# Performance work log

Measured on AMD Instinct MI355X. Metric: run time of the kernel, lower is better.

## Reference

```python
import jax, jax.numpy as jnp
import numpy as np

DEPTH = 64
N_HEAD = 8
FF = 128
EPS = 1e-5


def layer_norm(x, g, b):
    mu = jnp.mean(x, axis=-1, keepdims=True)
    var = jnp.mean((x - mu) ** 2, axis=-1, keepdims=True)
    return (x - mu) * jax.lax.rsqrt(var + EPS) * g + b


def setup_inputs() -> dict:
    key = jax.random.key(0)
    ks = jax.random.split(key, 16)
    B, S, d, h = 4, 512, DEPTH, N_HEAD
    s = 1.0 / np.sqrt(d)
    return {
        "seq": jax.random.normal(ks[0], (B, S, d), jnp.float32),
        "pos_enc": jax.random.normal(ks[1], (B, S, S, d), jnp.float32),
        "Wq": jax.random.normal(ks[2], (d, d * h), jnp.float32) * s,
        "Wk": jax.random.normal(ks[3], (d, d * h), jnp.float32) * s,
        "Wv": jax.random.normal(ks[4], (d, d * h), jnp.float32) * s,
        "Wo": jax.random.normal(ks[5], (d * h, d), jnp.float32) / np.sqrt(d * h),
        "Wp": jax.random.normal(ks[6], (d, h), jnp.float32) * s,
        "bp": jnp.zeros((h,), jnp.float32),
        "W1": jax.random.normal(ks[7], (d, FF), jnp.float32) * s,
        "b1": jnp.zeros((FF,), jnp.float32),
        "W2": jax.random.normal(ks[8], (FF, d), jnp.float32) / np.sqrt(FF),
        "b2": jnp.zeros((d,), jnp.float32),
        "g_att": jnp.ones((d,), jnp.float32),
        "b_att": jnp.zeros((d,), jnp.float32),
        "g_ff": jnp.ones((d,), jnp.float32),
        "b_ff": jnp.zeros((d,), jnp.float32),
    }


def reference(seq, pos_enc, Wq, Wk, Wv, Wo, Wp, bp, W1, b1, W2, b2, g_att, b_att, g_ff, b_ff):
    B, S, d = seq.shape
    h = N_HEAD
    # QKV: [B,S,h,d] -> [B,h,S,d]; head_dim == depth in this module
    q = (seq @ Wq).reshape(B, S, h, d).transpose(0, 2, 1, 3)
    k = (seq @ Wk).reshape(B, S, h, d).transpose(0, 2, 1, 3)
    v = (seq @ Wv).reshape(B, S, h, d).transpose(0, 2, 1, 3)
    a = jnp.einsum('bhid,bhjd->bhij', q, k) / jnp.sqrt(jnp.asarray(d, seq.dtype))
    # additive learned positional bias: [B,S,S,d] @ [d,h] -> [B,S,S,h] -> [B,h,S,S]
    p = jnp.einsum('bijd,dh->bhij', pos_enc, Wp) + bp[None, :, None, None]
    a = jax.nn.softmax(a + p, axis=-1)
    heads = jnp.einsum('bhij,bhjd->bhid', a, v)  # [B,h,S,d]
    o = heads.transpose(0, 2, 1, 3).reshape(B, S, h * d) @ Wo
    x = layer_norm(seq + o, g_att, b_att)
    y = jax.nn.relu(x @ W1 + b1) @ W2 + b2
    return layer_norm(x + y, g_ff, b_ff)
```

## Files before the change

kernel.cpp:

```cpp
#include <hip/hip_runtime.h>
#include <hip/hip_bf16.h>

#define DEPTH 64
#define NH 8
#define SEQL 512
#define BATCH 4
#define FFDIM 128
#define PROJ (DEPTH*NH)
#define LOG2E 1.44269504088896340736f

typedef __hip_bfloat16 bf16;
typedef __attribute__((ext_vector_type(8))) short short8;
typedef __attribute__((ext_vector_type(4))) float floatx4;

__device__ __forceinline__ short f2bs(float f) {
    __hip_bfloat16 h = __float2bfloat16(f);
    return *reinterpret_cast<short*>(&h);
}
__device__ __forceinline__ float bs2f(short s) {
    __hip_bfloat16 h = *reinterpret_cast<__hip_bfloat16*>(&s);
    return __bfloat162float(h);
}

__global__ __launch_bounds__(256) void front_kernel(
    const float* __restrict__ seq, const float* __restrict__ Wq,
    const float* __restrict__ Wk, const float* __restrict__ Wv,
    const float* __restrict__ pos, const float* __restrict__ Wp,
    const float* __restrict__ bp,
    bf16* __restrict__ q, bf16* __restrict__ k, bf16* __restrict__ vT,
    bf16* __restrict__ p)
{
    __shared__ __align__(16) union {
        struct { short sS[64][72]; short sW[128][72]; } g;
        struct { float sW2[4][132]; float sb[8]; } pb;
    } U;
    int t = threadIdx.x;
    int bid = blockIdx.x;

    if (bid < 384) {
        int lane = t & 63, w = t >> 6;
        int z = bid >> 7, rem = bid & 127;
        int mi = rem & 31, ni = rem >> 5;
        const float* W; int vflag = 0; bf16* out;
        if (z == 0)      { W = Wq; out = q; }
        else if (z == 1) { W = Wk; out = k; }
        else             { W = Wv; out = vT; vflag = 1; }
        int m0 = mi * 64;
        int n0 = ni * 128;

        for (int idx = t; idx < 4096; idx += 256) {
            int r = idx >> 6, kk = idx & 63;
            U.g.sS[r][kk] = f2bs(seq[(long)(m0 + r)*64 + kk]);
        }
        for (int idx = t; idx < 8192; idx += 256) {
            int kk = idx >> 7, n = idx & 127;
            U.g.sW[n][kk] = f2bs(W[kk*512 + n0 + n]);
        }
        __syncthreads();

        int ln = lane & 15, g4 = lane >> 4;
        int mt = w;
        floatx4 acc[2][4];
        #pragma unroll
        for (int nh = 0; nh < 2; nh++)
            #pragma unroll
            for (int nt = 0; nt < 4; nt++) acc[nh][nt] = (floatx4){0.f,0.f,0.f,0.f};
        #pragma unroll
        for (int ks = 0; ks < 2; ks++) {
            short8 af = *(const short8*)&U.g.sS[mt*16 + ln][ks*32 + g4*8];
            #pragma unroll
            for (int nh = 0; nh < 2; nh++)
                #pragma unroll
                for (int nt = 0; nt < 4; nt++) {
                    short8 bfv = *(const short8*)&U.g.sW[nh*64 + nt*16 + ln][ks*32 + g4*8];
                    acc[nh][nt] = __builtin_amdgcn_mfma_f32_16x16x32_bf16(af, bfv, acc[nh][nt], 0, 0, 0);
                }
        }

        if (!vflag) {
            #pragma unroll
            for (int nh = 0; nh < 2; nh++)
                #pragma unroll
                for (int nt = 0; nt < 4; nt++)
                    #pragma unroll
                    for (int r = 0; r < 4; r++) {
                        int grow = m0 + mt*16 + g4*4 + r;
                        int col  = n0 + nh*64 + nt*16 + ln;
                        int b = grow >> 9, s = grow & 511;
                        int h = col >> 6, d = col & 63;
                        out[(((long)(b*8 + h)*512) + s)*64 + d] = __float2bfloat16(acc[nh][nt][r]);
                    }
        } else {
            __syncthreads();
            short (*sT)[72] = U.g.sW;
            #pragma unroll
            for (int nh = 0; nh < 2; nh++)
                #pragma unroll
                for (int nt = 0; nt < 4; nt++)
                    #pragma unroll
                    for (int r = 0; r < 4; r++)
                        sT[nh*64 + nt*16 + ln][mt*16 + g4*4 + r] = f2bs(acc[nh][nt][r]);
            __syncthreads();
            int b = m0 >> 9, s0 = m0 & 511;
            for (int idx = t; idx < 1024; idx += 256) {
                int lc = idx >> 3, c8 = idx & 7;
                *(uint4*)(out + ((long)(b*512 + n0 + lc))*512 + s0 + c8*8) =
                    *(const uint4*)&sT[lc][c8*8];
            }
        }
    } else {
        int pid = bid - 384;
        for (int i = t; i < 512; i += 256) {
            int sub = i >> 7, rest = i & 127;
            int lk = rest >> 3, h = rest & 7;
            int kk = ((lk >> 2) << 4) + sub*4 + (lk & 3);
            U.pb.sW2[sub][lk*8 + h] = Wp[kk*8 + h];
        }
        if (t < 8) U.pb.sb[t] = bp[t];
        __syncthreads();

        int sub = t & 3;
        int lrow = t >> 2;
        long row = (long)pid*64 + lrow;

        const float4* src = (const float4*)(pos + row*64);
        float4 ch[4];
        #pragma unroll
        for (int i = 0; i < 4; i++) ch[i] = src[i*4 + sub];

        float acc[8];
        #pragma unroll
        for (int h = 0; h < 8; h++) acc[h] = 0.f;
        #pragma unroll
        for (int i = 0; i < 4; i++) {
            #pragma unroll
            for (int e = 0; e < 4; e++) {
                float x = ((const float*)&ch[i])[e];
                int lk = i*4 + e;
                const float4* wr = (const float4*)&U.pb.sW2[sub][lk*8];
                float4 wa = wr[0], wb = wr[1];
                acc[0] += x*wa.x; acc[1] += x*wa.y; acc[2] += x*wa.z; acc[3] += x*wa.w;
                acc[4] += x*wb.x; acc[5] += x*wb.y; acc[6] += x*wb.z; acc[7] += x*wb.w;
            }
        }
        #pragma unroll
        for (int h = 0; h < 8; h++) {
            acc[h] += __shfl_xor(acc[h], 1, 64);
            acc[h] += __shfl_xor(acc[h], 2, 64);
        }
        int b = (int)(row >> 18);
        int rem = (int)(row & 262143);
        int i = rem >> 9, j = rem & 511;
        int h1 = sub, h2 = sub + 4;
        p[(((long)(b*8 + h1)*512 + i) << 9) + j] = __float2bfloat16(acc[h1] + U.pb.sb[h1]);
        p[(((long)(b*8 + h2)*512 + i) << 9) + j] = __float2bfloat16(acc[h2] + U.pb.sb[h2]);
    }
}

__global__ __launch_bounds__(128) void attn_kernel(
    const bf16* __restrict__ q, const bf16* __restrict__ k,
    const bf16* __restrict__ vT, const bf16* __restrict__ p,
    bf16* __restrict__ heads)
{
    __shared__ __align__(16) short sQ[32*72];
    __shared__ __align__(16) short sK[64*72];
    __shared__ __align__(16) short sV[64*72];
    __shared__ __align__(16) short sP[2][16*72];

    int t = threadIdx.x;
    int lane = t & 63, w = t >> 6;
    int bid = blockIdx.x;
    int it = bid & 15;
    int bh = bid >> 4;
    int i0 = it*32;

    const bf16* qb = q + ((long)bh*SEQL + i0)*DEPTH;
    const bf16* kb = k + (long)bh*SEQL*DEPTH;
    const bf16* vb = vT + (long)bh*DEPTH*SEQL;
    const bf16* pb = p + ((long)bh*SEQL + i0)*SEQL;

    for (int c = t; c < 256; c += 128) {
        int r = c >> 3, c8 = c & 7;
        *(uint4*)((char*)sQ + r*144 + c8*16) = *(const uint4*)(qb + r*64 + c8*8);
    }

    int ln = lane & 15, g4 = lane >> 4;
    float lsum[4];
    floatx4 oacc[4];
    #pragma unroll
    for (int r = 0; r < 4; r++) lsum[r] = 0.f;
    #pragma unroll
    for (int ds = 0; ds < 4; ds++) oacc[ds] = (floatx4){0.f,0.f,0.f,0.f};

    unsigned short pf[16];
    #pragma unroll
    for (int js = 0; js < 4; js++)
        #pragma unroll
        for (int r = 0; r < 4; r++)
            pf[js*4 + r] = *(const unsigned short*)&pb[(long)(w*16 + g4*4 + r)*SEQL + js*16 + ln];

    #pragma unroll
    for (int jt = 0; jt < 8; jt++) {
        __syncthreads();
        int j0 = jt*64;
        for (int c = t; c < 512; c += 128) {
            int r = c >> 3, c8 = c & 7;
            *(uint4*)((char*)sK + r*144 + c8*16) = *(const uint4*)(kb + (long)(j0 + r)*64 + c8*8);
        }
        for (int c = t; c < 512; c += 128) {
            int r = c >> 3, c8 = c & 7;
            *(uint4*)((char*)sV + r*144 + c8*16) = *(const uint4*)(vb + (long)r*512 + j0 + c8*8);
        }
        __syncthreads();

        unsigned short cur[16];
        #pragma unroll
        for (int e = 0; e < 16; e++) cur[e] = pf[e];
        if (jt < 7) {
            int jn = (jt + 1)*64;
            #pragma unroll
            for (int js = 0; js < 4; js++)
                #pragma unroll
                for (int r = 0; r < 4; r++)
                    pf[js*4 + r] = *(const unsigned short*)&pb[(long)(w*16 + g4*4 + r)*SEQL + jn + js*16 + ln];
        }

        floatx4 sacc[4];
        #pragma unroll
        for (int js = 0; js < 4; js++) sacc[js] = (floatx4){0.f,0.f,0.f,0.f};
        #pragma unroll
        for (int kk = 0; kk < 2; kk++) {
            short8 aq = *(const short8*)((const char*)sQ + (w*16 + ln)*144 + kk*64 + g4*16);
            #pragma unroll
            for (int js = 0; js < 4; js++) {
                short8 bk = *(const short8*)((const char*)sK + (js*16 + ln)*144 + kk*64 + g4*16);
                sacc[js] = __builtin_amdgcn_mfma_f32_16x16x32_bf16(aq, bk, sacc[js], 0, 0, 0);
            }
        }
        #pragma unroll
        for (int js = 0; js < 4; js++)
            #pragma unroll
            for (int r = 0; r < 4; r++) {
                float pv = bs2f((short)cur[js*4 + r]);
                float e = exp2f((sacc[js][r]*0.125f + pv)*LOG2E);
                lsum[r] += e;
                sP[w][(g4*4 + r)*72 + js*16 + ln] = f2bs(e);
            }
        #pragma unroll
        for (int kk = 0; kk < 2; kk++) {
            short8 ap = *(const short8*)((const char*)sP[w] + ln*144 + kk*64 + g4*16);
            #pragma unroll
            for (int ds = 0; ds < 4; ds++) {
                short8 bv = *(const short8*)((const char*)sV + (ds*16 + ln)*144 + kk*64 + g4*16);
                oacc[ds] = __builtin_amdgcn_mfma_f32_16x16x32_bf16(ap, bv, oacc[ds], 0, 0, 0);
            }
        }
    }

    #pragma unroll
    for (int r = 0; r < 4; r++)
        #pragma unroll
        for (int m = 1; m < 16; m <<= 1) lsum[r] += __shfl_xor(lsum[r], m, 64);

    int b = bh >> 3, h = bh & 7;
    #pragma unroll
    for (int ds = 0; ds < 4; ds++)
        #pragma unroll
        for (int r = 0; r < 4; r++) {
            float val = oacc[ds][r] / lsum[r];
            int gi = i0 + w*16 + g4*4 + r;
            int col = h*64 + ds*16 + ln;
            heads[((long)b*SEQL + gi)*PROJ + col] = __float2bfloat16(val);
        }
}

__global__ __launch_bounds__(256) void tail_kernel(
    const bf16* __restrict__ heads, const float* __restrict__ Wo,
    const float* __restrict__ seq, const float* __restrict__ g_att,
    const float* __restrict__ b_att, const float* __restrict__ W1,
    const float* __restrict__ b1, const float* __restrict__ W2,
    const float* __restrict__ b2, const float* __restrict__ g_ff,
    const float* __restrict__ b_ff, float* __restrict__ out)
{
    __shared__ __align__(16) short sH[8][520];
    __shared__ float sX[8][68];
    __shared__ float sHid[8][132];
    int t = threadIdx.x;
    int w = t >> 6, lane = t & 63;
    long g0 = (long)blockIdx.x*8;

    for (int idx = t; idx < 512; idx += 256) {
        int r = idx >> 6, c8 = idx & 63;
        *(uint4*)((char*)&sH[r][0] + c8*16) = *(const uint4*)(heads + (g0 + r)*PROJ + c8*8);
    }
    __syncthreads();

    int r0 = w*2, r1 = w*2 + 1;
    float acc0 = 0.f, acc1 = 0.f;
    #pragma unroll 4
    for (int kk8 = 0; kk8 < 64; kk8++) {
        short8 a0 = *(const short8*)&sH[r0][kk8*8];
        short8 a1 = *(const short8*)&sH[r1][kk8*8];
        #pragma unroll
        for (int e = 0; e < 8; e++) {
            float wv = Wo[(kk8*8 + e)*DEPTH + lane];
            acc0 += bs2f(a0[e])*wv;
            acc1 += bs2f(a1[e])*wv;
        }
    }
    float ga = g_att[lane], ba = b_att[lane];
    float xn[2];
    #pragma unroll
    for (int rr = 0; rr < 2; rr++) {
        long row = g0 + w*2 + rr;
        float x0 = (rr ? acc1 : acc0) + seq[row*DEPTH + lane];
        float s1 = x0, s2 = x0*x0;
        #pragma unroll
        for (int m = 1; m < 64; m <<= 1) { s1 += __shfl_xor(s1, m, 64); s2 += __shfl_xor(s2, m, 64); }
        float mu = s1*(1.f/64.f);
        float var = s2*(1.f/64.f) - mu*mu;
        float rstd = rsqrtf(var + 1e-5f);
        xn[rr] = (x0 - mu)*rstd*ga + ba;
        sX[w*2 + rr][lane] = xn[rr];
    }

    float b1a = b1[lane], b1b = b1[lane + 64];
    float h00 = b1a, h01 = b1b, h10 = b1a, h11 = b1b;
    #pragma unroll 4
    for (int kk = 0; kk < DEPTH; kk++) {
        float w0 = W1[kk*FFDIM + lane];
        float w1 = W1[kk*FFDIM + 64 + lane];
        float x0v = sX[r0][kk], x1v = sX[r1][kk];
        h00 += x0v*w0; h01 += x0v*w1;
        h10 += x1v*w0; h11 += x1v*w1;
    }
    sHid[r0][lane] = fmaxf(h00, 0.f); sHid[r0][lane + 64] = fmaxf(h01, 0.f);
    sHid[r1][lane] = fmaxf(h10, 0.f); sHid[r1][lane + 64] = fmaxf(h11, 0.f);

    float bb = b2[lane];
    float acc20 = bb, acc21 = bb;
    #pragma unroll 4
    for (int kk = 0; kk < FFDIM; kk++) {
        float wv = W2[kk*DEPTH + lane];
        acc20 += sHid[r0][kk]*wv;
        acc21 += sHid[r1][kk]*wv;
    }
    float gf = g_ff[lane], bf = b_ff[lane];
    #pragma unroll
    for (int rr = 0; rr < 2; rr++) {
        long row = g0 + w*2 + rr;
        float z = xn[rr] + (rr ? acc21 : acc20);
        float t1 = z, t2 = z*z;
        #pragma unroll
        for (int m = 1; m < 64; m <<= 1) { t1 += __shfl_xor(t1, m, 64); t2 += __shfl_xor(t2, m, 64); }
        float mu2 = t1*(1.f/64.f);
        float var2 = t2*(1.f/64.f) - mu2*mu2;
        float rstd2 = rsqrtf(var2 + 1e-5f);
        out[row*DEPTH + lane] = (z - mu2)*rstd2*gf + bf;
    }
}

extern "C" void kernel_launch(void* const* d_in, const int* in_sizes, int n_in,
                              void* d_out, int out_size, void* d_ws, size_t ws_size,
                              hipStream_t stream) {
    const float* seq   = (const float*)d_in[0];
    const float* pos   = (const float*)d_in[1];
    const float* Wq    = (const float*)d_in[2];
    const float* Wk    = (const float*)d_in[3];
    const float* Wv    = (const float*)d_in[4];
    const float* Wo    = (const float*)d_in[5];
    const float* Wp    = (const float*)d_in[6];
    const float* bp    = (const float*)d_in[7];
    const float* W1    = (const float*)d_in[8];
    const float* b1    = (const float*)d_in[9];
    const float* W2    = (const float*)d_in[10];
    const float* b2    = (const float*)d_in[11];
    const float* g_att = (const float*)d_in[12];
    const float* b_att = (const float*)d_in[13];
    const float* g_ff  = (const float*)d_in[14];
    const float* b_ff  = (const float*)d_in[15];
    float* outp = (float*)d_out;

    bf16* qb  = (bf16*)d_ws;
    bf16* kb  = qb + 1048576;
    bf16* vTb = kb + 1048576;
    bf16* pb  = vTb + 1048576;
    bf16* hb  = pb + 8388608;

    front_kernel<<<16768, 256, 0, stream>>>(seq, Wq, Wk, Wv, pos, Wp, bp,
                                            qb, kb, vTb, pb);
    attn_kernel <<<512,   128, 0, stream>>>(qb, kb, vTb, pb, hb);
    tail_kernel <<<256,   256, 0, stream>>>(hb, Wo, seq, g_att, b_att,
                                            W1, b1, W2, b2, g_ff, b_ff, outp);
}
```

Measured before the change: 121.3 us.

## Split front kernel, store positional bias head-interleaved, widen attention tiles

Splits the fused front kernel into separate QKV and positional-bias kernels. The bias kernel now handles two rows per thread and writes all 8 heads as one 16-byte vector in a [B,S,S,h] layout, replacing scattered 2-byte stores. The attention kernel reads that interleaved layout with a stride of 8 and now uses 64-row query tiles with 4 waves. The aim is to cut the store cost of writing the large bias tensor. The trade-off is that attention gathers the bias with strided 2-byte loads, and there is one extra kernel launch.

```diff
diff --git a/kernel.cpp b/kernel.cpp
--- a/kernel.cpp
+++ b/kernel.cpp
@@ -22,164 +22,174 @@
     return __bfloat162float(h);
 }
 
-__global__ __launch_bounds__(256) void front_kernel(
+__global__ __launch_bounds__(256) void qkv_kernel(
     const float* __restrict__ seq, const float* __restrict__ Wq,
     const float* __restrict__ Wk, const float* __restrict__ Wv,
+    bf16* __restrict__ q, bf16* __restrict__ k, bf16* __restrict__ vT)
+{
+    __shared__ __align__(16) short sS[64][72];
+    __shared__ __align__(16) short sW[128][72];
+    __shared__ __align__(16) short sT[128][72];
+    int t = threadIdx.x;
+    int lane = t & 63, w = t >> 6;
+    const float* W; int vflag = 0;
+    bf16* out;
+    if (blockIdx.z == 0)      { W = Wq; out = q; }
+    else if (blockIdx.z == 1) { W = Wk; out = k; }
+    else                      { W = Wv; out = vT; vflag = 1; }
+    int m0 = blockIdx.x * 64;
+    int n0 = blockIdx.y * 128;
+
+    for (int idx = t; idx < 4096; idx += 256) {
+        int r = idx >> 6, kk = idx & 63;
+        sS[r][kk] = f2bs(seq[(long)(m0 + r)*64 + kk]);
+    }
+    for (int idx = t; idx < 8192; idx += 256) {
+        int kk = idx >> 7, n = idx & 127;
+        sW[n][kk] = f2bs(W[kk*512 + n0 + n]);
+    }
+    __syncthreads();
+
+    int ln = lane & 15, g4 = lane >> 4;
+    int mt = w;
+    floatx4 acc[2][4];
+    #pragma unroll
+    for (int nh = 0; nh < 2; nh++)
+        #pragma unroll
+        for (int nt = 0; nt < 4; nt++) acc[nh][nt] = (floatx4){0.f,0.f,0.f,0.f};
+    #pragma unroll
+    for (int ks = 0; ks < 2; ks++) {
+        short8 af = *(const short8*)&sS[mt*16 + ln][ks*32 + g4*8];
+        #pragma unroll
+        for (int nh = 0; nh < 2; nh++)
+            #pragma unroll
+            for (int nt = 0; nt < 4; nt++) {
+                short8 bfv = *(const short8*)&sW[nh*64 + nt*16 + ln][ks*32 + g4*8];
+                acc[nh][nt] = __builtin_amdgcn_mfma_f32_16x16x32_bf16(af, bfv, acc[nh][nt], 0, 0, 0);
+            }
+    }
+
+    if (!vflag) {
+        #pragma unroll
+        for (int nh = 0; nh < 2; nh++)
+            #pragma unroll
+            for (int nt = 0; nt < 4; nt++)
+                #pragma unroll
+                for (int r = 0; r < 4; r++) {
+                    int grow = m0 + mt*16 + g4*4 + r;
+                    int col  = n0 + nh*64 + nt*16 + ln;
+                    int b = grow >> 9, s = grow & 511;
+                    int h = col >> 6, d = col & 63;
+                    out[(((long)(b*8 + h)*512) + s)*64 + d] = __float2bfloat16(acc[nh][nt][r]);
+                }
+    } else {
+        #pragma unroll
+        for (int nh = 0; nh < 2; nh++)
+            #pragma unroll
+            for (int nt = 0; nt < 4; nt++)
+                #pragma unroll
+                for (int r = 0; r < 4; r++)
+                    sT[nh*64 + nt*16 + ln][mt*16 + g4*4 + r] = f2bs(acc[nh][nt][r]);
+        __syncthreads();
+        int b = m0 >> 9, s0 = m0 & 511;
+        for (int idx = t; idx < 1024; idx += 256) {
+            int lc = idx >> 3, c8 = idx & 7;
+            *(uint4*)(out + ((long)(b*512 + n0 + lc))*512 + s0 + c8*8) =
+                *(const uint4*)&sT[lc][c8*8];
+        }
+    }
+}
+
+__global__ __launch_bounds__(256, 8) void pbias_kernel(
     const float* __restrict__ pos, const float* __restrict__ Wp,
-    const float* __restrict__ bp,
-    bf16* __restrict__ q, bf16* __restrict__ k, bf16* __restrict__ vT,
-    bf16* __restrict__ p)
+    const float* __restrict__ bp, bf16* __restrict__ p)
 {
-    __shared__ __align__(16) union {
-        struct { short sS[64][72]; short sW[128][72]; } g;
-        struct { float sW2[4][132]; float sb[8]; } pb;
-    } U;
+    __shared__ __align__(16) float sW2[4][132];
+    __shared__ float sb[8];
     int t = threadIdx.x;
-    int bid = blockIdx.x;
-
-    if (bid < 384) {
-        int lane = t & 63, w = t >> 6;
-        int z = bid >> 7, rem = bid & 127;
-        int mi = rem & 31, ni = rem >> 5;
-        const float* W; int vflag = 0; bf16* out;
-        if (z == 0)      { W = Wq; out = q; }
-        else if (z == 1) { W = Wk; out = k; }
-        else             { W = Wv; out = vT; vflag = 1; }
-        int m0 = mi * 64;
-        int n0 = ni * 128;
-
-        for (int idx = t; idx < 4096; idx += 256) {
-            int r = idx >> 6, kk = idx & 63;
-            U.g.sS[r][kk] = f2bs(seq[(long)(m0 + r)*64 + kk]);
-        }
-        for (int idx = t; idx < 8192; idx += 256) {
-            int kk = idx >> 7, n = idx & 127;
-            U.g.sW[n][kk] = f2bs(W[kk*512 + n0 + n]);
-        }
-        __syncthreads();
-
-        int ln = lane & 15, g4 = lane >> 4;
-        int mt = w;
-        floatx4 acc[2][4];
-        #pragma unroll
-        for (int nh = 0; nh < 2; nh++)
-            #pragma unroll
-            for (int nt = 0; nt < 4; nt++) acc[nh][nt] = (floatx4){0.f,0.f,0.f,0.f};
-        #pragma unroll
-        for (int ks = 0; ks < 2; ks++) {
-            short8 af = *(const short8*)&U.g.sS[mt*16 + ln][ks*32 + g4*8];
-            #pragma unroll
-            for (int nh = 0; nh < 2; nh++)
-                #pragma unroll
-                for (int nt = 0; nt < 4; nt++) {
-                    short8 bfv = *(const short8*)&U.g.sW[nh*64 + nt*16 + ln][ks*32 + g4*8];
-                    acc[nh][nt] = __builtin_amdgcn_mfma_f32_16x16x32_bf16(af, bfv, acc[nh][nt], 0, 0, 0);
-                }
-        }
-
-        if (!vflag) {
-            #pragma unroll
-            for (int nh = 0; nh < 2; nh++)
-                #pragma unroll
-                for (int nt = 0; nt < 4; nt++)
-                    #pragma unroll
-                    for (int r = 0; r < 4; r++) {
-                        int grow = m0 + mt*16 + g4*4 + r;
-                        int col  = n0 + nh*64 + nt*16 + ln;
-                        int b = grow >> 9, s = grow & 511;
-                        int h = col >> 6, d = col & 63;
-                        out[(((long)(b*8 + h)*512) + s)*64 + d] = __float2bfloat16(acc[nh][nt][r]);
-                    }
-        } else {
-            __syncthreads();
-            short (*sT)[72] = U.g.sW;
-            #pragma unroll
-            for (int nh = 0; nh < 2; nh++)
-                #pragma unroll
-                for (int nt = 0; nt < 4; nt++)
-                    #pragma unroll
-                    for (int r = 0; r < 4; r++)
-                        sT[nh*64 + nt*16 + ln][mt*16 + g4*4 + r] = f2bs(acc[nh][nt][r]);
-            __syncthreads();
-            int b = m0 >> 9, s0 = m0 & 511;
-            for (int idx = t; idx < 1024; idx += 256) {
-                int lc = idx >> 3, c8 = idx & 7;
-                *(uint4*)(out + ((long)(b*512 + n0 + lc))*512 + s0 + c8*8) =
-                    *(const uint4*)&sT[lc][c8*8];
-            }
-        }
-    } else {
-        int pid = bid - 384;
-        for (int i = t; i < 512; i += 256) {
-            int sub = i >> 7, rest = i & 127;
-            int lk = rest >> 3, h = rest & 7;
-            int kk = ((lk >> 2) << 4) + sub*4 + (lk & 3);
-            U.pb.sW2[sub][lk*8 + h] = Wp[kk*8 + h];
-        }
-        if (t < 8) U.pb.sb[t] = bp[t];
-        __syncthreads();
-
-        int sub = t & 3;
-        int lrow = t >> 2;
-        long row = (long)pid*64 + lrow;
-
-        const float4* src = (const float4*)(pos + row*64);
-        float4 ch[4];
-        #pragma unroll
-        for (int i = 0; i < 4; i++) ch[i] = src[i*4 + sub];
-
-        float acc[8];
-        #pragma unroll
-        for (int h = 0; h < 8; h++) acc[h] = 0.f;
-        #pragma unroll
-        for (int i = 0; i < 4; i++) {
-            #pragma unroll
-            for (int e = 0; e < 4; e++) {
-                float x = ((const float*)&ch[i])[e];
-                int lk = i*4 + e;
-                const float4* wr = (const float4*)&U.pb.sW2[sub][lk*8];
-                float4 wa = wr[0], wb = wr[1];
-                acc[0] += x*wa.x; acc[1] += x*wa.y; acc[2] += x*wa.z; acc[3] += x*wa.w;
-                acc[4] += x*wb.x; acc[5] += x*wb.y; acc[6] += x*wb.z; acc[7] += x*wb.w;
-            }
-        }
+    for (int i = t; i < 512; i += 256) {
+        int sub = i >> 7, rest = i & 127;
+        int lk = rest >> 3, h = rest & 7;
+        int kk = ((lk >> 2) << 4) + sub*4 + (lk & 3);
+        sW2[sub][lk*8 + h] = Wp[kk*8 + h];
+    }
+    if (t < 8) sb[t] = bp[t];
+    __syncthreads();
+
+    int sub = t & 3;
+    int lr = t >> 2;
+    long rowA = (long)blockIdx.x*128 + lr;
+    long rowB = rowA + 64;
+
+    const float4* srcA = (const float4*)(pos + rowA*64);
+    const float4* srcB = (const float4*)(pos + rowB*64);
+    float4 chA[4], chB[4];
+    #pragma unroll
+    for (int i = 0; i < 4; i++) chA[i] = srcA[i*4 + sub];
+    #pragma unroll
+    for (int i = 0; i < 4; i++) chB[i] = srcB[i*4 + sub];
+
+    float accA[8], accB[8];
+    #pragma unroll
+    for (int h = 0; h < 8; h++) { accA[h] = 0.f; accB[h] = 0.f; }
+    #pragma unroll
+    for (int i = 0; i < 4; i++) {
+        #pragma unroll
+        for (int e = 0; e < 4; e++) {
+            int lk = i*4 + e;
+            const float4* wr = (const float4*)&sW2[sub][lk*8];
+            float4 wa = wr[0], wb = wr[1];
+            float xA = ((const float*)&chA[i])[e];
+            float xB = ((const float*)&chB[i])[e];
+            accA[0] += xA*wa.x; accA[1] += xA*wa.y; accA[2] += xA*wa.z; accA[3] += xA*wa.w;
+            accA[4] += xA*wb.x; accA[5] += xA*wb.y; accA[6] += xA*wb.z; accA[7] += xA*wb.w;
+            accB[0] += xB*wa.x; accB[1] += xB*wa.y; accB[2] += xB*wa.z; accB[3] += xB*wa.w;
+            accB[4] += xB*wb.x; accB[5] += xB*wb.y; accB[6] += xB*wb.z; accB[7] += xB*wb.w;
+        }
+    }
+    #pragma unroll
+    for (int h = 0; h < 8; h++) {
+        accA[h] += __shfl_xor(accA[h], 1, 64);
+        accA[h] += __shfl_xor(accA[h], 2, 64);
+        accB[h] += __shfl_xor(accB[h], 1, 64);
+        accB[h] += __shfl_xor(accB[h], 2, 64);
+    }
+    if (sub == 0) {
+        short8 vA, vB;
         #pragma unroll
         for (int h = 0; h < 8; h++) {
-            acc[h] += __shfl_xor(acc[h], 1, 64);
-            acc[h] += __shfl_xor(acc[h], 2, 64);
-        }
-        int b = (int)(row >> 18);
-        int rem = (int)(row & 262143);
-        int i = rem >> 9, j = rem & 511;
-        int h1 = sub, h2 = sub + 4;
-        p[(((long)(b*8 + h1)*512 + i) << 9) + j] = __float2bfloat16(acc[h1] + U.pb.sb[h1]);
-        p[(((long)(b*8 + h2)*512 + i) << 9) + j] = __float2bfloat16(acc[h2] + U.pb.sb[h2]);
-    }
-}
-
-__global__ __launch_bounds__(128) void attn_kernel(
+            vA[h] = f2bs(accA[h] + sb[h]);
+            vB[h] = f2bs(accB[h] + sb[h]);
+        }
+        *(short8*)(p + rowA*8) = vA;
+        *(short8*)(p + rowB*8) = vB;
+    }
+}
+
+__global__ __launch_bounds__(256) void attn_kernel(
     const bf16* __restrict__ q, const bf16* __restrict__ k,
     const bf16* __restrict__ vT, const bf16* __restrict__ p,
     bf16* __restrict__ heads)
 {
-    __shared__ __align__(16) short sQ[32*72];
+    __shared__ __align__(16) short sQ[64*72];
     __shared__ __align__(16) short sK[64*72];
     __shared__ __align__(16) short sV[64*72];
-    __shared__ __align__(16) short sP[2][16*72];
+    __shared__ __align__(16) short sP[4][16*72];
 
     int t = threadIdx.x;
     int lane = t & 63, w = t >> 6;
     int bid = blockIdx.x;
-    int it = bid & 15;
-    int bh = bid >> 4;
-    int i0 = it*32;
+    int it = bid & 7;
+    int bh = bid >> 3;
+    int i0 = it*64;
+    int b = bh >> 3, h = bh & 7;
 
     const bf16* qb = q + ((long)bh*SEQL + i0)*DEPTH;
     const bf16* kb = k + (long)bh*SEQL*DEPTH;
     const bf16* vb = vT + (long)bh*DEPTH*SEQL;
-    const bf16* pb = p + ((long)bh*SEQL + i0)*SEQL;
-
-    for (int c = t; c < 256; c += 128) {
+    const bf16* pb = p + (((long)b*512 + i0)*512)*8 + h;
+
+    for (int c = t; c < 512; c += 256) {
         int r = c >> 3, c8 = c & 7;
         *(uint4*)((char*)sQ + r*144 + c8*16) = *(const uint4*)(qb + r*64 + c8*8);
     }
@@ -197,17 +207,16 @@
     for (int js = 0; js < 4; js++)
         #pragma unroll
         for (int r = 0; r < 4; r++)
-            pf[js*4 + r] = *(const unsigned short*)&pb[(long)(w*16 + g4*4 + r)*SEQL + js*16 + ln];
-
-    #pragma unroll
+            pf[js*4 + r] = *(const unsigned short*)&pb[((long)(w*16 + g4*4 + r)*512 + js*16 + ln)*8];
+
     for (int jt = 0; jt < 8; jt++) {
         __syncthreads();
         int j0 = jt*64;
-        for (int c = t; c < 512; c += 128) {
+        for (int c = t; c < 512; c += 256) {
             int r = c >> 3, c8 = c & 7;
             *(uint4*)((char*)sK + r*144 + c8*16) = *(const uint4*)(kb + (long)(j0 + r)*64 + c8*8);
         }
-        for (int c = t; c < 512; c += 128) {
+        for (int c = t; c < 512; c += 256) {
             int r = c >> 3, c8 = c & 7;
             *(uint4*)((char*)sV + r*144 + c8*16) = *(const uint4*)(vb + (long)r*512 + j0 + c8*8);
         }
@@ -222,7 +231,7 @@
             for (int js = 0; js < 4; js++)
                 #pragma unroll
                 for (int r = 0; r < 4; r++)
-                    pf[js*4 + r] = *(const unsigned short*)&pb[(long)(w*16 + g4*4 + r)*SEQL + jn + js*16 + ln];
+                    pf[js*4 + r] = *(const unsigned short*)&pb[((long)(w*16 + g4*4 + r)*512 + jn + js*16 + ln)*8];
         }
 
         floatx4 sacc[4];
@@ -262,7 +271,6 @@
         #pragma unroll
         for (int m = 1; m < 16; m <<= 1) lsum[r] += __shfl_xor(lsum[r], m, 64);
 
-    int b = bh >> 3, h = bh & 7;
     #pragma unroll
     for (int ds = 0; ds < 4; ds++)
         #pragma unroll
@@ -387,9 +395,9 @@
     bf16* pb  = vTb + 1048576;
     bf16* hb  = pb + 8388608;
 
-    front_kernel<<<16768, 256, 0, stream>>>(seq, Wq, Wk, Wv, pos, Wp, bp,
-                                            qb, kb, vTb, pb);
-    attn_kernel <<<512,   128, 0, stream>>>(qb, kb, vTb, pb, hb);
-    tail_kernel <<<256,   256, 0, stream>>>(hb, Wo, seq, g_att, b_att,
-                                            W1, b1, W2, b2, g_ff, b_ff, outp);
-}
+    qkv_kernel  <<<dim3(32, 4, 3), 256, 0, stream>>>(seq, Wq, Wk, Wv, qb, kb, vTb);
+    pbias_kernel<<<8192,           256, 0, stream>>>(pos, Wp, bp, pb);
+    attn_kernel <<<256,            256, 0, stream>>>(qb, kb, vTb, pb, hb);
+    tail_kernel <<<256,            256, 0, stream>>>(hb, Wo, seq, g_att, b_att,
+                                                     W1, b1, W2, b2, g_ff, b_ff, outp);
+}
```

Result: faster. 113.6 us (-6.4%).
